# Performance work log

Hardware: AMD Instinct MI355X
Metric: run time of the kernel (lower is better)

## Reference

```python
import jax, jax.numpy as jnp
import numpy as np

B, S, E, H, FFN = 4, 1024, 1024, 16, 4096
D = E // H
EPS = 1e-5


def setup_inputs() -> dict:
    key = jax.random.key(0)
    ks = jax.random.split(key, 13)
    n = lambda k, shp, sc=1.0: jax.random.normal(k, shp, jnp.float32) * sc
    return {
        "x": n(ks[0], (B, S, E)),
        "wq": n(ks[1], (E, E), E ** -0.5),
        "wk": n(ks[2], (E, E), E ** -0.5),
        "wv": n(ks[3], (E, E), E ** -0.5),
        "phase": n(ks[4], (H, D)),  # nn.Parameter(torch.randn(H, d_k))
        "ln1_g": jnp.ones((E,), jnp.float32),
        "ln1_b": jnp.zeros((E,), jnp.float32),
        "ln2_g": jnp.ones((E,), jnp.float32),
        "ln2_b": jnp.zeros((E,), jnp.float32),
        "w1": n(ks[5], (FFN, E), E ** -0.5),
        "b1": n(ks[6], (FFN,), 0.02),
        "w2": n(ks[7], (E, FFN), FFN ** -0.5),
        "b2": n(ks[8], (E,), 0.02),
    }


def _layer_norm(x, g, b):
    mu = jnp.mean(x, -1, keepdims=True)
    xc = x - mu
    var = jnp.mean(xc * xc, -1, keepdims=True)  # biased, like torch LayerNorm
    return xc * jax.lax.rsqrt(var + EPS) * g + b


def reference(x, wq, wk, wv, phase, ln1_g, ln1_b, ln2_g, ln2_b, w1, b1, w2, b2):
    b_, s_, e_ = x.shape

    def proj(w):  # torch Linear: x @ w.T, then split heads -> [B,H,S,D]
        return jnp.einsum("bse,fe->bsf", x, w).reshape(b_, s_, H, D).transpose(0, 2, 1, 3)

    q, k, v = proj(wq), proj(wk), proj(wv)
    ph = jnp.exp(1j * phase)[None, :, None, :]  # [1,H,1,D] complex64
    qc, kc, vc = q * ph, k * ph, v * ph
    # complex QK^T (note: plain transpose, NOT conjugate, per source)
    scores = jnp.einsum("bhsd,bhtd->bhst", qc, kc) / jnp.sqrt(jnp.float32(D))
    # complex softmax: exp(z)/sum exp(z), stabilized by max of real part
    m = jnp.max(scores.real, -1, keepdims=True)
    ez = jnp.exp(scores - m)
    attn = ez / jnp.sum(ez, -1, keepdims=True)
    out = jnp.einsum("bhst,bhtd->bhsd", attn, vc).real  # take real part to re-enter real pipeline
    out = out.transpose(0, 2, 1, 3).reshape(b_, s_, e_)
    x1 = _layer_norm(x + out, ln1_g, ln1_b)
    h = jax.nn.relu(jnp.einsum("bse,fe->bsf", x1, w1) + b1)
    ffn = jnp.einsum("bsf,ef->bse", h, w2) + b2
    return _layer_norm(x1 + ffn, ln2_g, ln2_b)
```

## Files before the change

### kernel.cpp

```cpp
#include <hip/hip_runtime.h>

typedef unsigned short u16;
typedef unsigned int u32;
typedef u16 u16x4 __attribute__((ext_vector_type(4)));
typedef u16 u16x8 __attribute__((ext_vector_type(8)));
typedef u32 u32x2 __attribute__((ext_vector_type(2)));
typedef u32 u32x4 __attribute__((ext_vector_type(4)));
typedef float f32x4 __attribute__((ext_vector_type(4)));
typedef __bf16 bf16x8 __attribute__((ext_vector_type(8)));

#define B_N 4
#define S_N 1024
#define E_N 1024
#define H_N 16
#define D_N 64
#define F_N 4096
#define NTOK 4096

#define SCK 0.18033688011112042f
#define SSK 0.01989436788648692f

static __device__ __forceinline__ u16 f2bf(float f) {
  u32 u = __builtin_bit_cast(u32, f);
  return (u16)((u + 0x7fffu + ((u >> 16) & 1u)) >> 16);
}
static __device__ __forceinline__ float bf2f(u16 v) {
  return __builtin_bit_cast(float, ((u32)v) << 16);
}
static __device__ __forceinline__ f32x4 mfma16(u16x8 a, u16x8 b, f32x4 c) {
  return __builtin_amdgcn_mfma_f32_16x16x32_bf16(
      __builtin_bit_cast(bf16x8, a), __builtin_bit_cast(bf16x8, b), c, 0, 0, 0);
}
static __device__ __forceinline__ float exp2_hw(float x) {
  float r; asm("v_exp_f32 %0, %1" : "=v"(r) : "v"(x)); return r;
}
static __device__ __forceinline__ float sin_hw(float x) {
  float r; asm("v_sin_f32 %0, %1" : "=v"(r) : "v"(x)); return r;
}
static __device__ __forceinline__ float cos_hw(float x) {
  float r; asm("v_cos_f32 %0, %1" : "=v"(r) : "v"(x)); return r;
}
static __device__ __forceinline__ u32 cvtpk(float lo, float hi) {
  u32 r; asm("v_cvt_pk_bf16_f32 %0, %1, %2" : "=v"(r) : "v"(lo), "v"(hi)); return r;
}
#define GLOAD16(gp, lp)                                              \
  __builtin_amdgcn_global_load_lds(                                  \
      (const __attribute__((address_space(1))) void*)(gp),           \
      (__attribute__((address_space(3))) void*)(lp), 16, 0, 0)

__global__ __launch_bounds__(256) void cvt_all(
    const float* __restrict__ s0, u16* __restrict__ d0, int n0,
    const float* __restrict__ s1, u16* __restrict__ d1, int n1,
    const float* __restrict__ s2, u16* __restrict__ d2, int n2,
    const float* __restrict__ s3, u16* __restrict__ d3, int n3,
    const float* __restrict__ s4, u16* __restrict__ d4, int n4,
    const float* __restrict__ s5, u16* __restrict__ d5, int n5) {
  const int seg = blockIdx.y;
  const float* src; u16* dst; int n;
  switch (seg) {
    case 0: src = s0; dst = d0; n = n0; break;
    case 1: src = s1; dst = d1; n = n1; break;
    case 2: src = s2; dst = d2; n = n2; break;
    case 3: src = s3; dst = d3; n = n3; break;
    case 4: src = s4; dst = d4; n = n4; break;
    default: src = s5; dst = d5; n = n5; break;
  }
  int i = blockIdx.x * 256 + threadIdx.x;
  if (i < n) {
    float4 v = ((const float4*)src)[i];
    u16x4 o;
    o[0] = f2bf(v.x); o[1] = f2bf(v.y); o[2] = f2bf(v.z); o[3] = f2bf(v.w);
    ((u16x4*)dst)[i] = o;
  }
}

template <int MODE>
__global__ __launch_bounds__(512, 2) void gemm2p(
    const u16* __restrict__ A, const u16* __restrict__ B0,
    const u16* __restrict__ B1, const u16* __restrict__ B2, int strideK,
    u16* __restrict__ o0, u16* __restrict__ o1, u16* __restrict__ o2,
    const float* __restrict__ biasp) {
  __shared__ u16 SMEM[4][256 * 64];
  const int tid = threadIdx.x;
  const int lane = tid & 63, wv = tid >> 6;
  const int l15 = lane & 15, l4 = lane >> 4;
  const int wr = wv >> 2, wc = wv & 3;

  int lin = blockIdx.x;
  { const int q = (int)gridDim.x >> 3; lin = (lin & 7) * q + (lin >> 3); }
  int bxr, by, kc = 0, region = 0;
  const u16* Bsrc = B0;
  if constexpr (MODE == 0) {
    const int bx12 = lin % 12; by = lin / 12;
    region = bx12 >> 2; bxr = bx12 & 3;
    Bsrc = (region == 0) ? B0 : (region == 1) ? B1 : B2;
  } else if constexpr (MODE == 1) {
    bxr = lin & 15; by = lin >> 4;
  } else {
    bxr = lin & 3; by = (lin >> 2) & 15; kc = lin >> 6;
  }

  const u16* Ab = A + (size_t)(by * 256) * strideK + (size_t)kc * 1024;
  const u16* Bb = Bsrc + (size_t)(bxr * 256) * strideK + (size_t)kc * 1024;

  int srow[4], scs[4];
#pragma unroll
  for (int i = 0; i < 4; ++i) {
    const int c = (wv * 4 + i) * 64 + lane;
    srow[i] = c >> 3;
    scs[i] = (c & 7) ^ (srow[i] & 7);
  }
  auto stage = [&](int buf, int kt) {
#pragma unroll
    for (int i = 0; i < 4; ++i) {
      const size_t off = (size_t)srow[i] * strideK + kt * 64 + scs[i] * 8;
      GLOAD16(Ab + off, (char*)SMEM[buf] + (wv * 4 + i) * 1024);
      GLOAD16(Bb + off, (char*)SMEM[2 + buf] + (wv * 4 + i) * 1024);
    }
  };

  f32x4 z4 = {0.f, 0.f, 0.f, 0.f};
  f32x4 acc[8][4];
#pragma unroll
  for (int m = 0; m < 8; ++m)
#pragma unroll
    for (int n = 0; n < 4; ++n) acc[m][n] = z4;

  stage(0, 0);
  __syncthreads();

  const int KT = 16;
  int buf = 0;
#pragma unroll 1
  for (int t = 0; t < KT; ++t) {
    if (t + 1 < KT) stage(buf ^ 1, t + 1);
#pragma unroll
    for (int kp = 0; kp < 2; ++kp) {
      u16x8 afr[8], bfr[4];
#pragma unroll
      for (int m = 0; m < 8; ++m) {
        const int row = wr * 128 + m * 16 + l15;
        const int off = row * 128 + ((((kp << 2) | l4) ^ (row & 7)) << 4);
        afr[m] = *(const u16x8*)((const char*)SMEM[buf] + off);
      }
#pragma unroll
      for (int n = 0; n < 4; ++n) {
        const int row = wc * 64 + n * 16 + l15;
        const int off = row * 128 + ((((kp << 2) | l4) ^ (row & 7)) << 4);
        bfr[n] = *(const u16x8*)((const char*)SMEM[2 + buf] + off);
      }
      __builtin_amdgcn_s_setprio(1);
#pragma unroll
      for (int m = 0; m < 8; ++m)
#pragma unroll
        for (int n = 0; n < 4; ++n) acc[m][n] = mfma16(afr[m], bfr[n], acc[m][n]);
      __builtin_amdgcn_s_setprio(0);
    }
    if (t + 1 < KT) {
      __syncthreads();
      buf ^= 1;
    }
  }

  __syncthreads();
  u16* SM = &SMEM[0][0];
  float bvv[4];
  if constexpr (MODE == 1) {
#pragma unroll
    for (int n = 0; n < 4; ++n) bvv[n] = biasp[bxr * 256 + wc * 64 + n * 16 + l15];
  }
#pragma unroll
  for (int n = 0; n < 4; ++n)
#pragma unroll
    for (int m = 0; m < 8; ++m)
#pragma unroll
      for (int j = 0; j < 4; ++j) {
        const int row = wr * 128 + m * 16 + l4 * 4 + j;
        const int col = wc * 64 + n * 16 + l15;
        float v = acc[m][n][j];
        if constexpr (MODE == 1) v = fmaxf(v + bvv[n], 0.f);
        *(u16*)((char*)SM + row * 512 + ((((col >> 3) ^ (row & 31))) << 4) +
                (col & 7) * 2) = f2bf(v);
      }
  __syncthreads();
  if constexpr (MODE == 0) {
    u16* outb = (region == 0) ? o0 : (region == 1) ? o1 : o2;
#pragma unroll
    for (int i = 0; i < 16; ++i) {
      const int q = i * 512 + tid;
      const int row = q >> 5, c = q & 31;
      const u16x8 v = *(const u16x8*)((const char*)SM + row * 512 +
                                      ((c ^ (row & 31)) << 4));
      const int gr = by * 256 + row;
      const int gcol = bxr * 256 + c * 8;
      const int bI = gr >> 10, sI = gr & 1023;
      const int hI = gcol >> 6, dI = gcol & 63;
      *(u16x8*)(outb + (((size_t)(bI * H_N + hI)) * S_N + sI) * D_N + dI) = v;
    }
  } else if constexpr (MODE == 1) {
#pragma unroll
    for (int i = 0; i < 16; ++i) {
      const int q = i * 512 + tid;
      const int row = q >> 5, c = q & 31;
      const u16x8 v = *(const u16x8*)((const char*)SM + row * 512 +
                                      ((c ^ (row & 31)) << 4));
      *(u16x8*)(o0 + (size_t)(by * 256 + row) * F_N + bxr * 256 + c * 8) = v;
    }
  } else {
#pragma unroll
    for (int i = 0; i < 16; ++i) {
      const int q = i * 512 + tid;
      const int row = q >> 5, c = q & 31;
      const u16x8 v = *(const u16x8*)((const char*)SM + row * 512 +
                                      ((c ^ (row & 31)) << 4));
      const size_t gr = (size_t)kc * NTOK + by * 256 + row;
      *(u16x8*)(o0 + gr * E_N + bxr * 256 + c * 8) = v;
    }
  }
}

__global__ __launch_bounds__(512, 4) void attn_kernel(
    const u16* __restrict__ Qg, const u16* __restrict__ Kg,
    const u16* __restrict__ Vg, const float* __restrict__ phase,
    float* __restrict__ outp) {
  __shared__ u16 KS[64 * 64];
  __shared__ u16 VT[64 * 64];
  __shared__ u16 PreS[128 * 32], PimS[128 * 32];

  const int tid = threadIdx.x;
  const int lane = tid & 63, wv = tid >> 6;
  const int l15 = lane & 15, l4 = lane >> 4;
  const int qt = blockIdx.x, hh = blockIdx.y, bb = blockIdx.z;
  const size_t hoff = ((size_t)(bb * H_N + hh)) * (size_t)(S_N * D_N);
  const u16* K0 = Kg + hoff;
  const u16* V0 = Vg + hoff;
  const int qrow = wv * 16 + l15;

  u16x8 qcf[2], qsf[2];
#pragma unroll
  for (int ks = 0; ks < 2; ++ks) {
    const u16x8 qraw = *(const u16x8*)(
        Qg + hoff + (size_t)(qt * 128 + qrow) * D_N + ks * 32 + l4 * 8);
#pragma unroll
    for (int e = 0; e < 8; ++e) {
      const int d = ks * 32 + l4 * 8 + e;
      float sp, cp;
      __sincosf(2.f * phase[hh * 64 + d], &sp, &cp);
      const float qv = bf2f(qraw[e]);
      qcf[ks][e] = f2bf(qv * cp * SCK);
      qsf[ks][e] = f2bf(qv * sp * SSK);
    }
  }

  f32x4 z4 = {0.f, 0.f, 0.f, 0.f};
  f32x4 U1[4], U2[4];
#pragma unroll
  for (int db = 0; db < 4; ++db) { U1[db] = z4; U2[db] = z4; }
  float mm = -1e30f, zre = 0.f, zim = 0.f;

  const int srow = tid >> 3, sc16 = tid & 7;
  const int skoff = (srow * 128 + sc16 * 16) ^ ((srow & 7) << 4);

  u32x4 rk = *(const u32x4*)(K0 + (size_t)srow * 64 + sc16 * 8);
  u16x8 rv;
#pragma unroll
  for (int w = 0; w < 8; ++w) rv[w] = V0[(size_t)(wv * 8 + w) * 64 + lane];

  for (int kt = 0; kt < 16; ++kt) {
    *(u32x4*)((char*)KS + skoff) = rk;
#pragma unroll
    for (int w = 0; w < 8; ++w)
      *(u16*)((char*)VT + lane * 128 + ((wv ^ (lane & 7)) << 4) + w * 2) = rv[w];
    if (kt < 15) {
      rk = *(const u32x4*)(K0 + (size_t)((kt + 1) * 64 + srow) * 64 + sc16 * 8);
#pragma unroll
      for (int w = 0; w < 8; ++w)
        rv[w] = V0[(size_t)((kt + 1) * 64 + wv * 8 + w) * 64 + lane];
    }
    __syncthreads();

#pragma unroll
    for (int ts = 0; ts < 2; ++ts) {
      f32x4 sre[2], sim[2];
      sre[0] = z4; sre[1] = z4; sim[0] = z4; sim[1] = z4;
      __builtin_amdgcn_s_setprio(1);
#pragma unroll
      for (int tb = 0; tb < 2; ++tb) {
        const int trow = ts * 32 + tb * 16 + l15;
#pragma unroll
        for (int ks = 0; ks < 2; ++ks) {
          const int off = (trow * 128 + ks * 64 + (l4 << 4)) ^ ((trow & 7) << 4);
          u16x8 ak = *(const u16x8*)((const char*)KS + off);
          sre[tb] = mfma16(ak, qcf[ks], sre[tb]);
          sim[tb] = mfma16(ak, qsf[ks], sim[tb]);
        }
      }
      __builtin_amdgcn_s_setprio(0);

      float tm = fmaxf(fmaxf(fmaxf(sre[0][0], sre[0][1]), fmaxf(sre[0][2], sre[0][3])),
                       fmaxf(fmaxf(sre[1][0], sre[1][1]), fmaxf(sre[1][2], sre[1][3])));
      tm = fmaxf(tm, __shfl_xor(tm, 16));
      tm = fmaxf(tm, __shfl_xor(tm, 32));
      if (__ballot(tm > mm + 8.f) != 0ull) {
        const float mn = fmaxf(mm, tm);
        const float sc = exp2_hw(mm - mn);
        mm = mn;
        zre *= sc; zim *= sc;
#pragma unroll
        for (int db = 0; db < 4; ++db) { U1[db] *= sc; U2[db] *= sc; }
      }

#pragma unroll
      for (int tb = 0; tb < 2; ++tb) {
        float pc[4], ps[4];
#pragma unroll
        for (int j = 0; j < 4; ++j) {
          const float e = exp2_hw(sre[tb][j] - mm);
          const float sn = sin_hw(sim[tb][j]);
          const float cs = cos_hw(sim[tb][j]);
          pc[j] = e * cs; ps[j] = e * sn;
        }
        zre += (pc[0] + pc[1]) + (pc[2] + pc[3]);
        zim += (ps[0] + ps[1]) + (ps[2] + ps[3]);
        u32x2 wre = {cvtpk(pc[0], pc[1]), cvtpk(pc[2], pc[3])};
        u32x2 wim = {cvtpk(ps[0], ps[1]), cvtpk(ps[2], ps[3])};
        const int offp = (qrow * 64 + tb * 32 + l4 * 8) ^ (((qrow >> 1) & 3) << 4);
        *(u32x2*)((char*)PreS + offp) = wre;
        *(u32x2*)((char*)PimS + offp) = wim;
      }

      const int offp2 = (qrow * 64 + (l4 << 4)) ^ (((qrow >> 1) & 3) << 4);
      u16x8 bre = *(const u16x8*)((const char*)PreS + offp2);
      u16x8 bim = *(const u16x8*)((const char*)PimS + offp2);
      __builtin_amdgcn_s_setprio(1);
#pragma unroll
      for (int db = 0; db < 4; ++db) {
        const int dd = db * 16 + l15;
        const int offv = dd * 128 + ((((ts << 2) | l4) ^ (dd & 7)) << 4);
        u16x8 av = *(const u16x8*)((const char*)VT + offv);
        U1[db] = mfma16(av, bre, U1[db]);
        U2[db] = mfma16(av, bim, U2[db]);
      }
      __builtin_amdgcn_s_setprio(0);
    }
    __syncthreads();
  }

  float zr = zre, zi = zim;
  zr += __shfl_xor(zr, 16); zr += __shfl_xor(zr, 32);
  zi += __shfl_xor(zi, 16); zi += __shfl_xor(zi, 32);
  const float inv = 1.f / (zr * zr + zi * zi);
  const int q = qt * 128 + qrow;
  float* orow = outp + ((size_t)(bb * S_N + q)) * E_N + hh * 64;
#pragma unroll
  for (int db = 0; db < 4; ++db) {
    float4 o;
#pragma unroll
    for (int j = 0; j < 4; ++j) {
      const int d = db * 16 + l4 * 4 + j;
      float sp, cp;
      __sincosf(phase[hh * 64 + d], &sp, &cp);
      const float nre = cp * U1[db][j] - sp * U2[db][j];
      const float nim = sp * U1[db][j] + cp * U2[db][j];
      ((float*)&o)[j] = (nre * zr + nim * zi) * inv;
    }
    *(float4*)(orow + db * 16 + l4 * 4) = o;
  }
}

__global__ __launch_bounds__(256) void add_ln_kernel(
    const float* __restrict__ a, const float* __restrict__ r,
    const float* __restrict__ g, const float* __restrict__ be,
    u16* __restrict__ outb) {
  const int tid = threadIdx.x;
  const int row = blockIdx.x;
  const int lane = tid & 63, wv = tid >> 6;
  const float4 va = ((const float4*)(a + (size_t)row * 1024))[tid];
  const float4 vr = ((const float4*)(r + (size_t)row * 1024))[tid];
  float4 v;
  v.x = va.x + vr.x; v.y = va.y + vr.y; v.z = va.z + vr.z; v.w = va.w + vr.w;
  float s = v.x + v.y + v.z + v.w;
#pragma unroll
  for (int m = 1; m < 64; m <<= 1) s += __shfl_xor(s, m);
  __shared__ float red[8];
  if (lane == 0) red[wv] = s;
  __syncthreads();
  s = red[0] + red[1] + red[2] + red[3];
  const float mu = s * (1.f / 1024.f);
  float4 xc;
  xc.x = v.x - mu; xc.y = v.y - mu; xc.z = v.z - mu; xc.w = v.w - mu;
  float q = xc.x * xc.x + xc.y * xc.y + xc.z * xc.z + xc.w * xc.w;
#pragma unroll
  for (int m = 1; m < 64; m <<= 1) q += __shfl_xor(q, m);
  if (lane == 0) red[4 + wv] = q;
  __syncthreads();
  q = red[4] + red[5] + red[6] + red[7];
  const float rs = rsqrtf(q * (1.f / 1024.f) + 1e-5f);
  const float4 gg = ((const float4*)g)[tid];
  const float4 bb4 = ((const float4*)be)[tid];
  u16x4 ob;
  ob[0] = f2bf(xc.x * rs * gg.x + bb4.x);
  ob[1] = f2bf(xc.y * rs * gg.y + bb4.y);
  ob[2] = f2bf(xc.z * rs * gg.z + bb4.z);
  ob[3] = f2bf(xc.w * rs * gg.w + bb4.w);
  *(u16x4*)(outb + (size_t)row * 1024 + tid * 4) = ob;
}

__global__ __launch_bounds__(256) void add_ln4_kernel(
    const u16* __restrict__ part,
    const u16* __restrict__ resid,
    const float* __restrict__ bias,
    const float* __restrict__ g, const float* __restrict__ be,
    float* __restrict__ outp) {
  const int tid = threadIdx.x;
  const int row = blockIdx.x;
  const int lane = tid & 63, wv = tid >> 6;
  const float4 bv = ((const float4*)bias)[tid];
  float4 v = {bv.x, bv.y, bv.z, bv.w};
#pragma unroll
  for (int kc = 0; kc < 4; ++kc) {
    const u16x4 pp = *(const u16x4*)(part + ((size_t)kc * NTOK + row) * 1024 + tid * 4);
    v.x += bf2f(pp[0]); v.y += bf2f(pp[1]); v.z += bf2f(pp[2]); v.w += bf2f(pp[3]);
  }
  const u16x4 rr = *(const u16x4*)(resid + (size_t)row * 1024 + tid * 4);
  v.x += bf2f(rr[0]); v.y += bf2f(rr[1]); v.z += bf2f(rr[2]); v.w += bf2f(rr[3]);
  float s = v.x + v.y + v.z + v.w;
#pragma unroll
  for (int m = 1; m < 64; m <<= 1) s += __shfl_xor(s, m);
  __shared__ float red[8];
  if (lane == 0) red[wv] = s;
  __syncthreads();
  s = red[0] + red[1] + red[2] + red[3];
  const float mu = s * (1.f / 1024.f);
  float4 xc;
  xc.x = v.x - mu; xc.y = v.y - mu; xc.z = v.z - mu; xc.w = v.w - mu;
  float q = xc.x * xc.x + xc.y * xc.y + xc.z * xc.z + xc.w * xc.w;
#pragma unroll
  for (int m = 1; m < 64; m <<= 1) q += __shfl_xor(q, m);
  if (lane == 0) red[4 + wv] = q;
  __syncthreads();
  q = red[4] + red[5] + red[6] + red[7];
  const float rs = rsqrtf(q * (1.f / 1024.f) + 1e-5f);
  const float4 gg = ((const float4*)g)[tid];
  const float4 bb4 = ((const float4*)be)[tid];
  float4 o;
  o.x = xc.x * rs * gg.x + bb4.x;
  o.y = xc.y * rs * gg.y + bb4.y;
  o.z = xc.z * rs * gg.z + bb4.z;
  o.w = xc.w * rs * gg.w + bb4.w;
  ((float4*)(outp + (size_t)row * 1024))[tid] = o;
}

extern "C" void kernel_launch(void* const* d_in, const int* in_sizes, int n_in,
                              void* d_out, int out_size, void* d_ws, size_t ws_size,
                              hipStream_t stream) {
  (void)in_sizes; (void)n_in; (void)out_size; (void)ws_size;
  const float* x = (const float*)d_in[0];
  const float* wq = (const float*)d_in[1];
  const float* wk = (const float*)d_in[2];
  const float* wvp = (const float*)d_in[3];
  const float* phase = (const float*)d_in[4];
  const float* ln1g = (const float*)d_in[5];
  const float* ln1b = (const float*)d_in[6];
  const float* ln2g = (const float*)d_in[7];
  const float* ln2b = (const float*)d_in[8];
  const float* w1 = (const float*)d_in[9];
  const float* b1 = (const float*)d_in[10];
  const float* w2 = (const float*)d_in[11];
  const float* b2 = (const float*)d_in[12];
  float* outp = (float*)d_out;

  char* p = (char*)d_ws;
  auto alloc = [&](size_t n) -> char* {
    char* q = p;
    p += (n + 255) & ~(size_t)255;
    return q;
  };
  const size_t TOKE = (size_t)NTOK * E_N;
  u16* xb = (u16*)alloc(TOKE * 2);
  u16* wqb = (u16*)alloc((size_t)E_N * E_N * 2);
  u16* wkb = (u16*)alloc((size_t)E_N * E_N * 2);
  u16* wvb = (u16*)alloc((size_t)E_N * E_N * 2);
  u16* w1b = (u16*)alloc((size_t)F_N * E_N * 2);
  u16* w2b = (u16*)alloc((size_t)E_N * F_N * 2);
  u16* Qp  = (u16*)alloc(TOKE * 2);
  u16* pad = (u16*)alloc(TOKE * 2);
  u16* Kp  = (u16*)alloc(TOKE * 2);
  u16* Vp  = (u16*)alloc(TOKE * 2);
  u16* sp0 = (u16*)alloc(TOKE * 2);
  float* attn_o = (float*)alloc(TOKE * 4);
  alloc(TOKE * 2);
  (void)pad;
  u16* x1b = xb;
  u16* hb = Qp;
  u16* part = sp0;

  dim3 blk(256);
  cvt_all<<<dim3(4096, 6), blk, 0, stream>>>(
      x, xb, (int)(TOKE / 4),
      wq, wqb, E_N * E_N / 4,
      wk, wkb, E_N * E_N / 4,
      wvp, wvb, E_N * E_N / 4,
      w1, w1b, F_N * E_N / 4,
      w2, w2b, E_N * F_N / 4);

  gemm2p<0><<<dim3(192), dim3(512), 0, stream>>>(
      xb, wqb, wkb, wvb, E_N, Qp, Kp, Vp, nullptr);

  attn_kernel<<<dim3(8, 16, 4), dim3(512), 0, stream>>>(
      Qp, Kp, Vp, phase, attn_o);

  add_ln_kernel<<<dim3(NTOK), blk, 0, stream>>>(x, attn_o, ln1g, ln1b, x1b);

  gemm2p<1><<<dim3(256), dim3(512), 0, stream>>>(
      x1b, w1b, nullptr, nullptr, E_N, hb, nullptr, nullptr, b1);

  gemm2p<2><<<dim3(256), dim3(512), 0, stream>>>(
      hb, w2b, nullptr, nullptr, F_N, part, nullptr, nullptr, nullptr);

  add_ln4_kernel<<<dim3(NTOK), blk, 0, stream>>>(part, x1b, b2, ln2g, ln2b, outp);
}
```

Before: 187.1 us.

## Halve attention query tile to 64 rows and remap blocks across XCDs

The attention kernel now uses 256-thread blocks covering 64 query rows instead of 512 threads covering 128, which doubles the grid to 1024 blocks. Each thread loads two K chunks and two V row groups per tile to fill the shared K/V tiles. A 1D block index is remapped so that consecutive blocks, which land on different XCDs, are grouped by (batch, head), aiming for better L2 reuse of K/V. The cost is twice as many K/V tile loads overall and more staging work per thread, in exchange for better occupancy and load balance.

```diff
diff --git a/kernel.cpp b/kernel.cpp
--- a/kernel.cpp
+++ b/kernel.cpp
@@ -219,18 +219,22 @@
   }
 }
 
-__global__ __launch_bounds__(512, 4) void attn_kernel(
+__global__ __launch_bounds__(256, 4) void attn_kernel(
     const u16* __restrict__ Qg, const u16* __restrict__ Kg,
     const u16* __restrict__ Vg, const float* __restrict__ phase,
     float* __restrict__ outp) {
   __shared__ u16 KS[64 * 64];
   __shared__ u16 VT[64 * 64];
-  __shared__ u16 PreS[128 * 32], PimS[128 * 32];
+  __shared__ u16 PreS[64 * 32], PimS[64 * 32];
 
   const int tid = threadIdx.x;
   const int lane = tid & 63, wv = tid >> 6;
   const int l15 = lane & 15, l4 = lane >> 4;
-  const int qt = blockIdx.x, hh = blockIdx.y, bb = blockIdx.z;
+  const int L = blockIdx.x;
+  const int within = L >> 3;
+  const int qt = within & 15;
+  const int g = (L & 7) * 8 + (within >> 4);
+  const int hh = g & 15, bb = g >> 4;
   const size_t hoff = ((size_t)(bb * H_N + hh)) * (size_t)(S_N * D_N);
   const u16* K0 = Kg + hoff;
   const u16* V0 = Vg + hoff;
@@ -240,7 +244,7 @@
 #pragma unroll
   for (int ks = 0; ks < 2; ++ks) {
     const u16x8 qraw = *(const u16x8*)(
-        Qg + hoff + (size_t)(qt * 128 + qrow) * D_N + ks * 32 + l4 * 8);
+        Qg + hoff + (size_t)(qt * 64 + qrow) * D_N + ks * 32 + l4 * 8);
 #pragma unroll
     for (int e = 0; e < 8; ++e) {
       const int d = ks * 32 + l4 * 8 + e;
@@ -258,24 +262,41 @@
   for (int db = 0; db < 4; ++db) { U1[db] = z4; U2[db] = z4; }
   float mm = -1e30f, zre = 0.f, zim = 0.f;
 
-  const int srow = tid >> 3, sc16 = tid & 7;
-  const int skoff = (srow * 128 + sc16 * 16) ^ ((srow & 7) << 4);
-
-  u32x4 rk = *(const u32x4*)(K0 + (size_t)srow * 64 + sc16 * 8);
-  u16x8 rv;
-#pragma unroll
-  for (int w = 0; w < 8; ++w) rv[w] = V0[(size_t)(wv * 8 + w) * 64 + lane];
+  int kr[2], ksl[2], koff[2];
+#pragma unroll
+  for (int i = 0; i < 2; ++i) {
+    const int c = i * 256 + tid;
+    kr[i] = c >> 3; ksl[i] = c & 7;
+    koff[i] = (kr[i] * 128 + ksl[i] * 16) ^ ((kr[i] & 7) << 4);
+  }
+  u32x4 rk[2];
+  u16x8 rv0, rv1;
+#pragma unroll
+  for (int i = 0; i < 2; ++i)
+    rk[i] = *(const u32x4*)(K0 + (size_t)kr[i] * 64 + ksl[i] * 8);
+#pragma unroll
+  for (int w = 0; w < 8; ++w) {
+    rv0[w] = V0[(size_t)(wv * 16 + w) * 64 + lane];
+    rv1[w] = V0[(size_t)(wv * 16 + 8 + w) * 64 + lane];
+  }
 
   for (int kt = 0; kt < 16; ++kt) {
-    *(u32x4*)((char*)KS + skoff) = rk;
-#pragma unroll
-    for (int w = 0; w < 8; ++w)
-      *(u16*)((char*)VT + lane * 128 + ((wv ^ (lane & 7)) << 4) + w * 2) = rv[w];
+#pragma unroll
+    for (int i = 0; i < 2; ++i) *(u32x4*)((char*)KS + koff[i]) = rk[i];
+#pragma unroll
+    for (int w = 0; w < 8; ++w) {
+      *(u16*)((char*)VT + lane * 128 + (((wv * 2) ^ (lane & 7)) << 4) + w * 2) = rv0[w];
+      *(u16*)((char*)VT + lane * 128 + (((wv * 2 + 1) ^ (lane & 7)) << 4) + w * 2) = rv1[w];
+    }
     if (kt < 15) {
-      rk = *(const u32x4*)(K0 + (size_t)((kt + 1) * 64 + srow) * 64 + sc16 * 8);
-#pragma unroll
-      for (int w = 0; w < 8; ++w)
-        rv[w] = V0[(size_t)((kt + 1) * 64 + wv * 8 + w) * 64 + lane];
+#pragma unroll
+      for (int i = 0; i < 2; ++i)
+        rk[i] = *(const u32x4*)(K0 + (size_t)((kt + 1) * 64 + kr[i]) * 64 + ksl[i] * 8);
+#pragma unroll
+      for (int w = 0; w < 8; ++w) {
+        rv0[w] = V0[(size_t)((kt + 1) * 64 + wv * 16 + w) * 64 + lane];
+        rv1[w] = V0[(size_t)((kt + 1) * 64 + wv * 16 + 8 + w) * 64 + lane];
+      }
     }
     __syncthreads();
 
@@ -350,7 +371,7 @@
   zr += __shfl_xor(zr, 16); zr += __shfl_xor(zr, 32);
   zi += __shfl_xor(zi, 16); zi += __shfl_xor(zi, 32);
   const float inv = 1.f / (zr * zr + zi * zi);
-  const int q = qt * 128 + qrow;
+  const int q = qt * 64 + qrow;
   float* orow = outp + ((size_t)(bb * S_N + q)) * E_N + hh * 64;
 #pragma unroll
   for (int db = 0; db < 4; ++db) {
@@ -507,7 +528,7 @@
   gemm2p<0><<<dim3(192), dim3(512), 0, stream>>>(
       xb, wqb, wkb, wvb, E_N, Qp, Kp, Vp, nullptr);
 
-  attn_kernel<<<dim3(8, 16, 4), dim3(512), 0, stream>>>(
+  attn_kernel<<<dim3(1024), dim3(256), 0, stream>>>(
       Qp, Kp, Vp, phase, attn_o);
 
   add_ln_kernel<<<dim3(NTOK), blk, 0, stream>>>(x, attn_o, ln1g, ln1b, x1b);
```

Measured after the change: 191.0 us. 2.1% more time.

## Emit V pre-transposed from QKV GEMM and remap attention block order

Applied to the files above, without the earlier changes.

The QKV projection epilogue now writes the V tile transposed (head, d, seq) by swapping row/col in the shared-memory staging. The attention kernel can then load V with one 16-byte vector load per thread and store it to LDS with the same swizzle as K, replacing eight scalar 2-byte global loads and eight scalar LDS stores per tile. The attention grid is also flattened and remapped so consecutive blocks are spread across heads/batches, which changes cache and XCD locality. The transposed epilogue writes 16-byte chunks along the sequence axis, so its global store pattern differs from the Q/K path.

```diff
diff --git a/kernel.cpp b/kernel.cpp
--- a/kernel.cpp
+++ b/kernel.cpp
@@ -169,6 +169,7 @@
 #pragma unroll
     for (int n = 0; n < 4; ++n) bvv[n] = biasp[bxr * 256 + wc * 64 + n * 16 + l15];
   }
+  const bool vtile = (MODE == 0) && (region == 2);
 #pragma unroll
   for (int n = 0; n < 4; ++n)
 #pragma unroll
@@ -179,23 +180,40 @@
         const int col = wc * 64 + n * 16 + l15;
         float v = acc[m][n][j];
         if constexpr (MODE == 1) v = fmaxf(v + bvv[n], 0.f);
-        *(u16*)((char*)SM + row * 512 + ((((col >> 3) ^ (row & 31))) << 4) +
-                (col & 7) * 2) = f2bf(v);
+        const int fr = vtile ? col : row;
+        const int fc = vtile ? row : col;
+        *(u16*)((char*)SM + fr * 512 + ((((fc >> 3) ^ (fr & 31))) << 4) +
+                (fc & 7) * 2) = f2bf(v);
       }
   __syncthreads();
   if constexpr (MODE == 0) {
-    u16* outb = (region == 0) ? o0 : (region == 1) ? o1 : o2;
-#pragma unroll
-    for (int i = 0; i < 16; ++i) {
-      const int q = i * 512 + tid;
-      const int row = q >> 5, c = q & 31;
-      const u16x8 v = *(const u16x8*)((const char*)SM + row * 512 +
-                                      ((c ^ (row & 31)) << 4));
-      const int gr = by * 256 + row;
-      const int gcol = bxr * 256 + c * 8;
-      const int bI = gr >> 10, sI = gr & 1023;
-      const int hI = gcol >> 6, dI = gcol & 63;
-      *(u16x8*)(outb + (((size_t)(bI * H_N + hI)) * S_N + sI) * D_N + dI) = v;
+    if (region == 2) {
+#pragma unroll
+      for (int i = 0; i < 16; ++i) {
+        const int q = i * 512 + tid;
+        const int crow = q >> 5, slot = q & 31;
+        const u16x8 v = *(const u16x8*)((const char*)SM + crow * 512 +
+                                        ((slot ^ (crow & 31)) << 4));
+        const int ch = bxr * 256 + crow;
+        const int hI = ch >> 6, dI = ch & 63;
+        const int tok = by * 256 + slot * 8;
+        const int bI = tok >> 10, sI = tok & 1023;
+        *(u16x8*)(o2 + (((size_t)(bI * H_N + hI)) * D_N + dI) * S_N + sI) = v;
+      }
+    } else {
+      u16* outb = (region == 0) ? o0 : o1;
+#pragma unroll
+      for (int i = 0; i < 16; ++i) {
+        const int q = i * 512 + tid;
+        const int row = q >> 5, c = q & 31;
+        const u16x8 v = *(const u16x8*)((const char*)SM + row * 512 +
+                                        ((c ^ (row & 31)) << 4));
+        const int gr = by * 256 + row;
+        const int gcol = bxr * 256 + c * 8;
+        const int bI = gr >> 10, sI = gr & 1023;
+        const int hI = gcol >> 6, dI = gcol & 63;
+        *(u16x8*)(outb + (((size_t)(bI * H_N + hI)) * S_N + sI) * D_N + dI) = v;
+      }
     }
   } else if constexpr (MODE == 1) {
 #pragma unroll
@@ -221,7 +239,7 @@
 
 __global__ __launch_bounds__(512, 4) void attn_kernel(
     const u16* __restrict__ Qg, const u16* __restrict__ Kg,
-    const u16* __restrict__ Vg, const float* __restrict__ phase,
+    const u16* __restrict__ Vtg, const float* __restrict__ phase,
     float* __restrict__ outp) {
   __shared__ u16 KS[64 * 64];
   __shared__ u16 VT[64 * 64];
@@ -230,10 +248,14 @@
   const int tid = threadIdx.x;
   const int lane = tid & 63, wv = tid >> 6;
   const int l15 = lane & 15, l4 = lane >> 4;
-  const int qt = blockIdx.x, hh = blockIdx.y, bb = blockIdx.z;
+  const int L = blockIdx.x;
+  const int within = L >> 3;
+  const int qt = within & 7;
+  const int g = (L & 7) * 8 + (within >> 3);
+  const int hh = g & 15, bb = g >> 4;
   const size_t hoff = ((size_t)(bb * H_N + hh)) * (size_t)(S_N * D_N);
   const u16* K0 = Kg + hoff;
-  const u16* V0 = Vg + hoff;
+  const u16* Vt0 = Vtg + hoff;
   const int qrow = wv * 16 + l15;
 
   u16x8 qcf[2], qsf[2];
@@ -258,24 +280,18 @@
   for (int db = 0; db < 4; ++db) { U1[db] = z4; U2[db] = z4; }
   float mm = -1e30f, zre = 0.f, zim = 0.f;
 
-  const int srow = tid >> 3, sc16 = tid & 7;
-  const int skoff = (srow * 128 + sc16 * 16) ^ ((srow & 7) << 4);
-
-  u32x4 rk = *(const u32x4*)(K0 + (size_t)srow * 64 + sc16 * 8);
-  u16x8 rv;
-#pragma unroll
-  for (int w = 0; w < 8; ++w) rv[w] = V0[(size_t)(wv * 8 + w) * 64 + lane];
+  const int krow = tid >> 3, kslot = tid & 7;
+  const int loff = (krow * 128 + kslot * 16) ^ ((krow & 7) << 4);
+
+  u32x4 rk = *(const u32x4*)(K0 + (size_t)krow * 64 + kslot * 8);
+  u32x4 rv = *(const u32x4*)(Vt0 + (size_t)krow * S_N + kslot * 8);
 
   for (int kt = 0; kt < 16; ++kt) {
-    *(u32x4*)((char*)KS + skoff) = rk;
-#pragma unroll
-    for (int w = 0; w < 8; ++w)
-      *(u16*)((char*)VT + lane * 128 + ((wv ^ (lane & 7)) << 4) + w * 2) = rv[w];
+    *(u32x4*)((char*)KS + loff) = rk;
+    *(u32x4*)((char*)VT + loff) = rv;
     if (kt < 15) {
-      rk = *(const u32x4*)(K0 + (size_t)((kt + 1) * 64 + srow) * 64 + sc16 * 8);
-#pragma unroll
-      for (int w = 0; w < 8; ++w)
-        rv[w] = V0[(size_t)((kt + 1) * 64 + wv * 8 + w) * 64 + lane];
+      rk = *(const u32x4*)(K0 + (size_t)((kt + 1) * 64 + krow) * 64 + kslot * 8);
+      rv = *(const u32x4*)(Vt0 + (size_t)krow * S_N + (kt + 1) * 64 + kslot * 8);
     }
     __syncthreads();
 
@@ -289,7 +305,7 @@
         const int trow = ts * 32 + tb * 16 + l15;
 #pragma unroll
         for (int ks = 0; ks < 2; ++ks) {
-          const int off = (trow * 128 + ks * 64 + (l4 << 4)) ^ ((trow & 7) << 4);
+          const int off = trow * 128 + ((((ks << 2) | l4) ^ (trow & 7)) << 4);
           u16x8 ak = *(const u16x8*)((const char*)KS + off);
           sre[tb] = mfma16(ak, qcf[ks], sre[tb]);
           sim[tb] = mfma16(ak, qsf[ks], sim[tb]);
@@ -486,7 +502,7 @@
   u16* Qp  = (u16*)alloc(TOKE * 2);
   u16* pad = (u16*)alloc(TOKE * 2);
   u16* Kp  = (u16*)alloc(TOKE * 2);
-  u16* Vp  = (u16*)alloc(TOKE * 2);
+  u16* Vtp = (u16*)alloc(TOKE * 2);
   u16* sp0 = (u16*)alloc(TOKE * 2);
   float* attn_o = (float*)alloc(TOKE * 4);
   alloc(TOKE * 2);
@@ -505,10 +521,10 @@
       w2, w2b, E_N * F_N / 4);
 
   gemm2p<0><<<dim3(192), dim3(512), 0, stream>>>(
-      xb, wqb, wkb, wvb, E_N, Qp, Kp, Vp, nullptr);
-
-  attn_kernel<<<dim3(8, 16, 4), dim3(512), 0, stream>>>(
-      Qp, Kp, Vp, phase, attn_o);
+      xb, wqb, wkb, wvb, E_N, Qp, Kp, Vtp, nullptr);
+
+  attn_kernel<<<dim3(512), dim3(512), 0, stream>>>(
+      Qp, Kp, Vtp, phase, attn_o);
 
   add_ln_kernel<<<dim3(NTOK), blk, 0, stream>>>(x, attn_o, ln1g, ln1b, x1b);
 
```

Result: no change. 188.6 us (+0.8%).
